# Kernel optimization log

Hardware: AMD Instinct MI355X
Metric: run time of the kernel (lower is better)

Reference implementation:

```python
import jax, jax.numpy as jnp
import numpy as np

NEG_SLOPE = 0.2  # PyG GATConv default negative_slope


def gat_conv(x, src, dst, W, a_src, a_dst, b):
    """PyG GATConv with concat=False (mean over heads). src/dst include self-loops."""
    N = x.shape[0]
    H, C = a_src.shape
    h = (x @ W).reshape(N, H, C)                      # [N,H,C]
    alpha_src = (h * a_src).sum(-1)                   # [N,H]
    alpha_dst = (h * a_dst).sum(-1)                   # [N,H]
    e = jax.nn.leaky_relu(alpha_src[src] + alpha_dst[dst], NEG_SLOPE)  # [E,H]
    # segment softmax over incoming edges of each dst node
    emax = jax.ops.segment_max(e, dst, num_segments=N)                 # [N,H]
    ex = jnp.exp(e - emax[dst])                                        # [E,H]
    denom = jax.ops.segment_sum(ex, dst, num_segments=N)               # [N,H]
    alpha = ex / denom[dst]                                            # [E,H]
    msg = h[src] * alpha[:, :, None]                                   # [E,H,C]
    out = jax.ops.segment_sum(msg, dst, num_segments=N)                # [N,H,C]
    return out.mean(axis=1) + b                                        # concat=False -> mean heads


def setup_inputs() -> dict:
    key = jax.random.key(0)
    ks = jax.random.split(key, 16)
    N, F_IN, H, C, E = 50000, 3, 4, 64, 800000
    inp = {
        "x": jax.random.normal(ks[0], (N, F_IN), dtype=jnp.float32),
        "edge_index": jax.random.randint(ks[1], (2, E), 0, N, dtype=jnp.int32),
        "W1": jax.random.normal(ks[2], (F_IN, H * C), dtype=jnp.float32) * 0.1,
        "a1_src": jax.random.normal(ks[3], (H, C), dtype=jnp.float32) * 0.1,
        "a1_dst": jax.random.normal(ks[4], (H, C), dtype=jnp.float32) * 0.1,
        "b1": jnp.zeros((C,), dtype=jnp.float32),
        "W2": jax.random.normal(ks[5], (C, H * C), dtype=jnp.float32) * 0.1,
        "a2_src": jax.random.normal(ks[6], (H, C), dtype=jnp.float32) * 0.1,
        "a2_dst": jax.random.normal(ks[7], (H, C), dtype=jnp.float32) * 0.1,
        "b2": jnp.zeros((C,), dtype=jnp.float32),
        "W3": jax.random.normal(ks[8], (C, H * C), dtype=jnp.float32) * 0.1,
        "a3_src": jax.random.normal(ks[9], (H, C), dtype=jnp.float32) * 0.1,
        "a3_dst": jax.random.normal(ks[10], (H, C), dtype=jnp.float32) * 0.1,
        "b3": jnp.zeros((C,), dtype=jnp.float32),
        "lin_w": jax.random.normal(ks[11], (C, 1), dtype=jnp.float32) * 0.1,
        "lin_b": jnp.zeros((1,), dtype=jnp.float32),
    }
    return inp


def reference(x, edge_index, W1, a1_src, a1_dst, b1, W2, a2_src, a2_dst, b2,
              W3, a3_src, a3_dst, b3, lin_w, lin_b):
    N = x.shape[0]
    loops = jnp.arange(N, dtype=edge_index.dtype)  # PyG add_self_loops=True default
    src = jnp.concatenate([edge_index[0], loops])
    dst = jnp.concatenate([edge_index[1], loops])

    h1 = jax.nn.elu(gat_conv(x, src, dst, W1, a1_src, a1_dst, b1))
    h2 = jax.nn.elu(gat_conv(h1, src, dst, W2, a2_src, a2_dst, b2)) + h1
    h3 = jax.nn.elu(gat_conv(h2, src, dst, W3, a3_src, a3_dst, b3)) + h2
    return h3 @ lin_w + lin_b
```

## Files before the change

### kernel.cpp

```cpp
#include <hip/hip_runtime.h>
#include <math.h>

#define HEADS 4
#define CH 64
#define HC 256

typedef __attribute__((ext_vector_type(8))) short bf16x8;
typedef __attribute__((ext_vector_type(4))) float f32x4;

__device__ __forceinline__ float lrelu(float v) { return v > 0.f ? v : 0.2f * v; }

__device__ __forceinline__ unsigned int f2bf(float f) {
    unsigned int u = __float_as_uint(f);
    u += 0x7fffu + ((u >> 16) & 1u);
    return u >> 16;
}
__device__ __forceinline__ float bf2f(unsigned short u) {
    return __uint_as_float(((unsigned int)u) << 16);
}

__device__ __forceinline__ float4 wave_sum4(float4 v) {
#pragma unroll
    for (int m = 32; m; m >>= 1) {
        v.x += __shfl_xor(v.x, m);
        v.y += __shfl_xor(v.y, m);
        v.z += __shfl_xor(v.z, m);
        v.w += __shfl_xor(v.w, m);
    }
    return v;
}

__global__ void count_kernel(const int* __restrict__ dst, int E, int vec_ok,
                             float scale8, int* __restrict__ deg) {
    int r = blockIdx.x & 7;
    int i = (blockIdx.x >> 3) * blockDim.x + threadIdx.x;
    int e0 = i * 4;
    if (e0 >= E) return;
    int d[4];
    int cnt;
    if (vec_ok && e0 + 3 < E) {
        int4 v = *(const int4*)(dst + e0);
        d[0] = v.x; d[1] = v.y; d[2] = v.z; d[3] = v.w; cnt = 4;
    } else {
        cnt = min(4, E - e0);
        for (int k = 0; k < cnt; ++k) d[k] = dst[e0 + k];
    }
    for (int k = 0; k < cnt; ++k) {
        int rr = min(7, (int)((float)d[k] * scale8));
        if (rr == r) atomicAdd(&deg[d[k]], 1);
    }
}

__global__ void scan_blocks(const int* __restrict__ deg,
                            int* __restrict__ off,
                            int* __restrict__ bsum,
                            const float* __restrict__ x,
                            float4* __restrict__ xq, int N) {
    __shared__ int sh[256];
    int t = threadIdx.x;
    int g = blockIdx.x * 256 + t;
    int v = (g < N) ? deg[g] + 1 : 0;
    if (g < N) xq[g] = make_float4(x[3 * g], x[3 * g + 1], x[3 * g + 2], 0.f);
    sh[t] = v;
    __syncthreads();
    for (int d = 1; d < 256; d <<= 1) {
        int xv = (t >= d) ? sh[t - d] : 0;
        __syncthreads();
        sh[t] += xv;
        __syncthreads();
    }
    if (g < N) off[g] = sh[t] - v;
    if (t == 255) bsum[blockIdx.x] = sh[255];
}

__global__ void scan_bsums(int* __restrict__ bsum, int G,
                           int* __restrict__ total_out) {
    __shared__ int sh[256];
    int t = threadIdx.x;
    int chunk = (G + 255) / 256;
    int lo = t * chunk, hi = min(lo + chunk, G);
    int s = 0;
    for (int i = lo; i < hi; ++i) s += bsum[i];
    sh[t] = s;
    __syncthreads();
    for (int d = 1; d < 256; d <<= 1) {
        int xv = (t >= d) ? sh[t - d] : 0;
        __syncthreads();
        sh[t] += xv;
        __syncthreads();
    }
    int run = (t > 0) ? sh[t - 1] : 0;
    for (int i = lo; i < hi; ++i) { int v = bsum[i]; bsum[i] = run; run += v; }
    if (t == 255) *total_out = sh[255];
}

__global__ void scan_add(int* __restrict__ off, const int* __restrict__ bsum,
                         const int* __restrict__ deg,
                         int* __restrict__ csr_src, int N) {
    int g = blockIdx.x * 256 + threadIdx.x;
    if (g < N) {
        int o = off[g] + bsum[blockIdx.x];
        off[g] = o;
        csr_src[o + deg[g]] = g;
    }
}

__global__ void scatter_kernel(const int* __restrict__ src,
                               const int* __restrict__ dst, int E, int vec_ok,
                               float scale8,
                               const int* __restrict__ off,
                               int* __restrict__ cursor,
                               int* __restrict__ csr_src) {
    int r = blockIdx.x & 7;
    int i = (blockIdx.x >> 3) * blockDim.x + threadIdx.x;
    int e0 = i * 4;
    if (e0 >= E) return;
    int s[4], d[4];
    int cnt;
    if (vec_ok && e0 + 3 < E) {
        int4 sv = *(const int4*)(src + e0);
        int4 dv = *(const int4*)(dst + e0);
        s[0] = sv.x; s[1] = sv.y; s[2] = sv.z; s[3] = sv.w;
        d[0] = dv.x; d[1] = dv.y; d[2] = dv.z; d[3] = dv.w; cnt = 4;
    } else {
        cnt = min(4, E - e0);
        for (int k = 0; k < cnt; ++k) { s[k] = src[e0 + k]; d[k] = dst[e0 + k]; }
    }
    for (int k = 0; k < cnt; ++k) {
        int rr = min(7, (int)((float)d[k] * scale8));
        if (rr != r) continue;
        int p = atomicAdd(&cursor[d[k]], 1);
        csr_src[off[d[k]] + p] = s[k];
    }
}

__device__ __forceinline__ void prep_blk(int b, int t, const float* W,
                                         const float* a_s, const float* a_d,
                                         unsigned short* Wb, float* ws,
                                         float* wd) {
    if (b < 64) {
        Wb[b * 256 + t] = (unsigned short)f2bf(W[(t >> 2) * HC + (t & 3) * CH + b]);
    } else {
        int idx = (b - 64) * 256 + t;
        int which = idx >= 256;
        int i = which ? idx - 256 : idx;
        int k = i >> 2, h = i & 3;
        const float* av = (which ? a_d : a_s) + h * CH;
        const float* Wr = W + (size_t)k * HC + h * CH;
        float s = 0.f;
        for (int c = 0; c < CH; ++c) s += Wr[c] * av[c];
        (which ? wd : ws)[i] = s;
    }
}

__global__ void prep_all(const float* __restrict__ W1,
                         const float* __restrict__ a1s,
                         const float* __restrict__ a1d,
                         float* __restrict__ ws1, float* __restrict__ wd1,
                         const float* __restrict__ W2,
                         const float* __restrict__ a2s,
                         const float* __restrict__ a2d,
                         unsigned short* __restrict__ Wb2,
                         float* __restrict__ ws2, float* __restrict__ wd2,
                         const float* __restrict__ W3,
                         const float* __restrict__ a3s,
                         const float* __restrict__ a3d,
                         unsigned short* __restrict__ Wb3,
                         float* __restrict__ ws3, float* __restrict__ wd3) {
    int b = blockIdx.x, t = threadIdx.x;
    if (b < 66) {
        prep_blk(b, t, W2, a2s, a2d, Wb2, ws2, wd2);
    } else if (b < 132) {
        prep_blk(b - 66, t, W3, a3s, a3d, Wb3, ws3, wd3);
    } else {
        for (int idx = t; idx < 24; idx += blockDim.x) {
            int which = idx >= 12;
            int i = which ? idx - 12 : idx;
            int k = i >> 2, h = i & 3;
            const float* av = (which ? a1d : a1s) + h * CH;
            const float* Wr = W1 + (size_t)k * HC + h * CH;
            float s = 0.f;
            for (int c = 0; c < CH; ++c) s += Wr[c] * av[c];
            (which ? wd1 : ws1)[i] = s;
        }
    }
}

__global__ void agg_kernel(const int* __restrict__ off,
                           const int* __restrict__ csr_src,
                           const unsigned short* __restrict__ xp,
                           const float4* __restrict__ asrc4,
                           const float4* __restrict__ adst4,
                           uint2* __restrict__ zb2, int N) {
    __shared__ float4 exs[4][64];
    __shared__ unsigned int sss[4][64];
    int node = (blockIdx.x * blockDim.x + threadIdx.x) >> 6;
    int w = (threadIdx.x >> 6) & 3;
    int lane = threadIdx.x & 63;
    if (node >= N) return;
    int o0 = off[node], o1 = off[node + 1];
    int deg = o1 - o0;
    float4 ad = adst4[node];

    float l0 = 0.f, l1 = 0.f, l2 = 0.f, l3 = 0.f;
    float z0 = 0.f, z1 = 0.f, z2 = 0.f, z3 = 0.f;
    const char* xpb = (const char*)xp + lane * 2;

    for (int base = 0; base < deg; base += 64) {
        int i = base + lane;
        int s = 0;
        float4 ev = make_float4(-INFINITY, -INFINITY, -INFINITY, -INFINITY);
        if (i < deg) {
            s = csr_src[o0 + i];
            float4 as = asrc4[s];
            ev.x = lrelu(as.x + ad.x);
            ev.y = lrelu(as.y + ad.y);
            ev.z = lrelu(as.z + ad.z);
            ev.w = lrelu(as.w + ad.w);
        }
        float4 ex;
        ex.x = __expf(ev.x);
        ex.y = __expf(ev.y);
        ex.z = __expf(ev.z);
        ex.w = __expf(ev.w);
        float4 ls = wave_sum4(ex);
        l0 += ls.x; l1 += ls.y; l2 += ls.z; l3 += ls.w;
        exs[w][lane] = ex;
        sss[w][lane] = (unsigned)s * 128u;

        int cnt = min(64, deg - base);
#pragma unroll 4
        for (int e = 0; e < cnt; ++e) {
            unsigned soff = sss[w][e];
            float4 exe = exs[w][e];
            float xk = bf2f(*(const unsigned short*)(xpb + soff));
            z0 += exe.x * xk; z1 += exe.y * xk;
            z2 += exe.z * xk; z3 += exe.w * xk;
        }
    }
    float s0 = 0.25f / l0, s1 = 0.25f / l1, s2 = 0.25f / l2, s3 = 0.25f / l3;
    uint2 zo;
    zo.x = f2bf(z0 * s0) | (f2bf(z1 * s1) << 16);
    zo.y = f2bf(z2 * s2) | (f2bf(z3 * s3) << 16);
    zb2[(size_t)node * CH + lane] = zo;
}

__global__ void gemm_mfma(const unsigned short* __restrict__ zb,
                          const unsigned short* __restrict__ Wb,
                          const float* __restrict__ bias,
                          const float* __restrict__ residual,
                          const float4* __restrict__ wsn4,
                          const float4* __restrict__ wdn4,
                          float4* __restrict__ asrc4,
                          float4* __restrict__ adst4,
                          const float* __restrict__ lin_w,
                          const float* __restrict__ lin_b,
                          float* __restrict__ out_f32,
                          unsigned short* __restrict__ out_pack,
                          float* __restrict__ out_final, int N) {
    int w = threadIdx.x >> 6;
    int lane = threadIdx.x & 63;
    int quad = lane >> 4, col = lane & 15;
    int nbase = blockIdx.x * 64 + w * 16;

    f32x4 zero4 = {0.f, 0.f, 0.f, 0.f};
    f32x4 acc[4];
#pragma unroll
    for (int t = 0; t < 4; ++t) acc[t] = zero4;

    const unsigned short* arow = zb + (size_t)(nbase + col) * HC + quad * 8;
#pragma unroll
    for (int q = 0; q < 8; ++q) {
        bf16x8 af = *(const bf16x8*)(arow + q * 32);
#pragma unroll
        for (int t = 0; t < 4; ++t) {
            const unsigned short* bp = Wb + (size_t)(t * 16 + col) * HC + q * 32 + quad * 8;
            bf16x8 bfrag = *(const bf16x8*)bp;
            acc[t] = __builtin_amdgcn_mfma_f32_16x16x32_bf16(af, bfrag, acc[t], 0, 0, 0);
        }
    }

    if (!out_final) {
        float vv[4][4];
#pragma unroll
        for (int t = 0; t < 4; ++t) {
            int c = t * 16 + col;
            float bc = bias[c];
#pragma unroll
            for (int r = 0; r < 4; ++r) {
                int n = nbase + quad * 4 + r;
                float v = acc[t][r] + bc;
                v = v > 0.f ? v : expm1f(v);
                v += residual[(size_t)n * CH + c];
                vv[t][r] = v;
                if (n < N) {
                    out_f32[(size_t)n * CH + c] = v;
                    out_pack[(size_t)n * CH + c] = (unsigned short)f2bf(v);
                }
            }
        }
        float4 wsv[4], wdv[4];
#pragma unroll
        for (int t = 0; t < 4; ++t) { wsv[t] = wsn4[t * 16 + col]; wdv[t] = wdn4[t * 16 + col]; }
#pragma unroll
        for (int r = 0; r < 4; ++r) {
            int n = nbase + quad * 4 + r;
            float4 sa = make_float4(0.f, 0.f, 0.f, 0.f);
            float4 da = make_float4(0.f, 0.f, 0.f, 0.f);
#pragma unroll
            for (int t = 0; t < 4; ++t) {
                float v = vv[t][r];
                sa.x += v * wsv[t].x; sa.y += v * wsv[t].y;
                sa.z += v * wsv[t].z; sa.w += v * wsv[t].w;
                da.x += v * wdv[t].x; da.y += v * wdv[t].y;
                da.z += v * wdv[t].z; da.w += v * wdv[t].w;
            }
#pragma unroll
            for (int m = 8; m; m >>= 1) {
                sa.x += __shfl_xor(sa.x, m); sa.y += __shfl_xor(sa.y, m);
                sa.z += __shfl_xor(sa.z, m); sa.w += __shfl_xor(sa.w, m);
                da.x += __shfl_xor(da.x, m); da.y += __shfl_xor(da.y, m);
                da.z += __shfl_xor(da.z, m); da.w += __shfl_xor(da.w, m);
            }
            if (col == 0 && n < N) { asrc4[n] = sa; adst4[n] = da; }
        }
    } else {
        float lw[4], bb[4];
#pragma unroll
        for (int t = 0; t < 4; ++t) { lw[t] = lin_w[t * 16 + col]; bb[t] = bias[t * 16 + col]; }
#pragma unroll
        for (int r = 0; r < 4; ++r) {
            int n = nbase + quad * 4 + r;
            float ts = 0.f;
#pragma unroll
            for (int t = 0; t < 4; ++t) {
                float v = acc[t][r] + bb[t];
                v = v > 0.f ? v : expm1f(v);
                v += residual[(size_t)n * CH + (t * 16 + col)];
                ts += v * lw[t];
            }
            ts += __shfl_xor(ts, 1);
            ts += __shfl_xor(ts, 2);
            ts += __shfl_xor(ts, 4);
            ts += __shfl_xor(ts, 8);
            if (col == 0 && n < N) out_final[n] = ts + lin_b[0];
        }
    }
}

__global__ void fused1_kernel(const int* __restrict__ off,
                              const int* __restrict__ csr_src,
                              const float4* __restrict__ xq,
                              const float* __restrict__ ws,
                              const float* __restrict__ wd,
                              float4* __restrict__ zl, int N) {
    int t = blockIdx.x * blockDim.x + threadIdx.x;
    int n = t >> 2, j = t & 3;
    if (n >= N) return;
    float4 xn = xq[n];
    float ad0 = xn.x * wd[0] + xn.y * wd[4] + xn.z * wd[8];
    float ad1 = xn.x * wd[1] + xn.y * wd[5] + xn.z * wd[9];
    float ad2 = xn.x * wd[2] + xn.y * wd[6] + xn.z * wd[10];
    float ad3 = xn.x * wd[3] + xn.y * wd[7] + xn.z * wd[11];

    int o0 = off[n], o1 = off[n + 1];
    float z[12];
#pragma unroll
    for (int q = 0; q < 12; ++q) z[q] = 0.f;
    float l0 = 0.f, l1 = 0.f, l2 = 0.f, l3 = 0.f;

    for (int i = o0 + j; i < o1; i += 4) {
        int s = csr_src[i];
        float4 xv = xq[s];
        float e0 = __expf(lrelu(xv.x * ws[0] + xv.y * ws[4] + xv.z * ws[8]  + ad0));
        float e1 = __expf(lrelu(xv.x * ws[1] + xv.y * ws[5] + xv.z * ws[9]  + ad1));
        float e2 = __expf(lrelu(xv.x * ws[2] + xv.y * ws[6] + xv.z * ws[10] + ad2));
        float e3 = __expf(lrelu(xv.x * ws[3] + xv.y * ws[7] + xv.z * ws[11] + ad3));
        l0 += e0; l1 += e1; l2 += e2; l3 += e3;
        z[0] += e0 * xv.x; z[1]  += e0 * xv.y; z[2]  += e0 * xv.z;
        z[3] += e1 * xv.x; z[4]  += e1 * xv.y; z[5]  += e1 * xv.z;
        z[6] += e2 * xv.x; z[7]  += e2 * xv.y; z[8]  += e2 * xv.z;
        z[9] += e3 * xv.x; z[10] += e3 * xv.y; z[11] += e3 * xv.z;
    }
#pragma unroll
    for (int m = 1; m < 4; m <<= 1) {
#pragma unroll
        for (int q = 0; q < 12; ++q) z[q] += __shfl_xor(z[q], m);
        l0 += __shfl_xor(l0, m);
        l1 += __shfl_xor(l1, m);
        l2 += __shfl_xor(l2, m);
        l3 += __shfl_xor(l3, m);
    }
    if (j == 0) {
        zl[(size_t)n * 4 + 0] = make_float4(z[0], z[1], z[2], z[3]);
        zl[(size_t)n * 4 + 1] = make_float4(z[4], z[5], z[6], z[7]);
        zl[(size_t)n * 4 + 2] = make_float4(z[8], z[9], z[10], z[11]);
        zl[(size_t)n * 4 + 3] = make_float4(l0, l1, l2, l3);
    }
}

__global__ void epi1_kernel(const float4* __restrict__ zl,
                            const float* __restrict__ W1,
                            const float* __restrict__ b1,
                            const float4* __restrict__ ws2_4,
                            const float4* __restrict__ wd2_4,
                            float4* __restrict__ asrc4,
                            float4* __restrict__ adst4,
                            float* __restrict__ out,
                            unsigned short* __restrict__ out_pack, int N) {
    int node = (blockIdx.x * blockDim.x + threadIdx.x) >> 6;
    int c = threadIdx.x & 63;
    if (node >= N) return;
    float4 z0 = zl[(size_t)node * 4 + 0];
    float4 z1 = zl[(size_t)node * 4 + 1];
    float4 z2 = zl[(size_t)node * 4 + 2];
    float4 l4 = zl[(size_t)node * 4 + 3];
    float i0 = 0.25f / l4.x, i1 = 0.25f / l4.y;
    float i2 = 0.25f / l4.z, i3 = 0.25f / l4.w;
    float acc =
        (z0.x * W1[0 * HC +   0 + c] + z0.y * W1[1 * HC +   0 + c] + z0.z * W1[2 * HC +   0 + c]) * i0 +
        (z0.w * W1[0 * HC +  64 + c] + z1.x * W1[1 * HC +  64 + c] + z1.y * W1[2 * HC +  64 + c]) * i1 +
        (z1.z * W1[0 * HC + 128 + c] + z1.w * W1[1 * HC + 128 + c] + z2.x * W1[2 * HC + 128 + c]) * i2 +
        (z2.y * W1[0 * HC + 192 + c] + z2.z * W1[1 * HC + 192 + c] + z2.w * W1[2 * HC + 192 + c]) * i3;
    float v = acc + b1[c];
    v = v > 0.f ? v : expm1f(v);
    out[(size_t)node * CH + c] = v;
    out_pack[(size_t)node * CH + c] = (unsigned short)f2bf(v);
    float4 wsv = ws2_4[c], wdv = wd2_4[c];
    float4 sacc = make_float4(v * wsv.x, v * wsv.y, v * wsv.z, v * wsv.w);
    float4 dacc = make_float4(v * wdv.x, v * wdv.y, v * wdv.z, v * wdv.w);
    sacc = wave_sum4(sacc);
    dacc = wave_sum4(dacc);
    if (c == 0) { asrc4[node] = sacc; adst4[node] = dacc; }
}

extern "C" void kernel_launch(void* const* d_in, const int* in_sizes, int n_in,
                              void* d_out, int out_size, void* d_ws, size_t ws_size,
                              hipStream_t stream) {
    const float* x      = (const float*)d_in[0];
    const int*   ei     = (const int*)  d_in[1];
    const float* W1     = (const float*)d_in[2];
    const float* a1s    = (const float*)d_in[3];
    const float* a1d    = (const float*)d_in[4];
    const float* b1     = (const float*)d_in[5];
    const float* W2     = (const float*)d_in[6];
    const float* a2s    = (const float*)d_in[7];
    const float* a2d    = (const float*)d_in[8];
    const float* b2     = (const float*)d_in[9];
    const float* W3     = (const float*)d_in[10];
    const float* a3s    = (const float*)d_in[11];
    const float* a3d    = (const float*)d_in[12];
    const float* b3     = (const float*)d_in[13];
    const float* lin_w  = (const float*)d_in[14];
    const float* lin_b  = (const float*)d_in[15];

    const int N = in_sizes[0] / 3;
    const int E = in_sizes[1] / 2;
    const int Et = E + N;
    const int* src = ei;
    const int* dst = ei + E;
    const float scale8 = 8.0f / (float)N;
    const int vec_ok = ((((size_t)src | (size_t)dst) & 15) == 0) ? 1 : 0;

    float* xq_f   = (float*)d_ws;
    unsigned short* zb  = (unsigned short*)(xq_f + (size_t)N * 4);
    unsigned short* xpA = zb  + (size_t)N * HC;
    unsigned short* xpB = xpA + (size_t)N * CH;
    unsigned short* Wb2 = xpB + (size_t)N * CH;
    unsigned short* Wb3 = Wb2 + 16384;
    float* bufA   = (float*)(Wb3 + 16384);
    float* bufB   = bufA + (size_t)N * CH;
    float* zl     = bufB + (size_t)N * CH;
    float* asrc   = zl   + (size_t)N * 16;
    float* adst   = asrc + (size_t)N * 4;
    float* ws1    = adst + (size_t)N * 4;
    float* wd1    = ws1 + 16;
    float* ws2    = wd1 + 16;
    float* wd2    = ws2 + 256;
    float* ws3    = wd2 + 256;
    float* wd3    = ws3 + 256;
    int* deg      = (int*)(wd3 + 256);
    int* cursor   = deg + N;
    int* off      = cursor + N;
    int* bsum     = off + N + 4;
    int* csr_src  = bsum + 256;

    const int B = 256;
    const int G = (N + 255) / 256;
    const int EB4 = (E + 3) / 4;
    const int CB = (EB4 + B - 1) / B;

    hipMemsetAsync(deg, 0, (size_t)2 * N * sizeof(int), stream);
    count_kernel<<<CB * 8, B, 0, stream>>>(dst, E, vec_ok, scale8, deg);
    scan_blocks<<<G, B, 0, stream>>>(deg, off, bsum, x, (float4*)xq_f, N);
    scan_bsums<<<1, B, 0, stream>>>(bsum, G, off + N);
    scan_add<<<G, B, 0, stream>>>(off, bsum, deg, csr_src, N);
    scatter_kernel<<<CB * 8, B, 0, stream>>>(src, dst, E, vec_ok, scale8,
                                             off, cursor, csr_src);

    prep_all<<<133, B, 0, stream>>>(W1, a1s, a1d, ws1, wd1,
                                    W2, a2s, a2d, Wb2, ws2, wd2,
                                    W3, a3s, a3d, Wb3, ws3, wd3);

    int nwave_blocks = (N * 64 + B - 1) / B;
    int ngemm_blocks = (N + 63) / 64;

    fused1_kernel<<<(N * 4 + B - 1) / B, B, 0, stream>>>(
        off, csr_src, (const float4*)xq_f, ws1, wd1, (float4*)zl, N);
    epi1_kernel<<<nwave_blocks, B, 0, stream>>>(
        (const float4*)zl, W1, b1, (const float4*)ws2, (const float4*)wd2,
        (float4*)asrc, (float4*)adst, bufA, xpA, N);

    agg_kernel<<<nwave_blocks, B, 0, stream>>>(
        off, csr_src, xpA, (const float4*)asrc, (const float4*)adst,
        (uint2*)zb, N);
    gemm_mfma<<<ngemm_blocks, B, 0, stream>>>(
        zb, Wb2, b2, bufA, (const float4*)ws3, (const float4*)wd3,
        (float4*)asrc, (float4*)adst,
        nullptr, nullptr, bufB, xpB, nullptr, N);

    agg_kernel<<<nwave_blocks, B, 0, stream>>>(
        off, csr_src, xpB, (const float4*)asrc, (const float4*)adst,
        (uint2*)zb, N);
    gemm_mfma<<<ngemm_blocks, B, 0, stream>>>(
        zb, Wb3, b3, bufB, nullptr, nullptr, nullptr, nullptr,
        lin_w, lin_b, nullptr, nullptr, (float*)d_out, N);
}
```

Measured before the change: 344.5 us.

## Reuse count atomics for CSR scatter, fuse layer-1 epilogue, split agg edges across half-waves

The count kernel now stores each edge's atomic slot, so the scatter becomes a plain non-atomic single-pass write instead of an 8-way partitioned atomic pass. The layer-1 aggregation and its epilogue (W1 projection, ELU, attention logits) merge into one kernel, removing the intermediate buffer and a launch. The aggregation kernel processes two edges per step across half-waves with 32-bit two-channel loads, then combines the halves with a shuffle. The cost is an extra E-sized slot array and more registers per lane in aggregation.

```diff
diff --git a/kernel.cpp b/kernel.cpp
--- a/kernel.cpp
+++ b/kernel.cpp
@@ -31,7 +31,8 @@
 }
 
 __global__ void count_kernel(const int* __restrict__ dst, int E, int vec_ok,
-                             float scale8, int* __restrict__ deg) {
+                             float scale8, int* __restrict__ deg,
+                             int* __restrict__ slot) {
     int r = blockIdx.x & 7;
     int i = (blockIdx.x >> 3) * blockDim.x + threadIdx.x;
     int e0 = i * 4;
@@ -47,7 +48,7 @@
     }
     for (int k = 0; k < cnt; ++k) {
         int rr = min(7, (int)((float)d[k] * scale8));
-        if (rr == r) atomicAdd(&deg[d[k]], 1);
+        if (rr == r) slot[e0 + k] = atomicAdd(&deg[d[k]], 1);
     }
 }
 
@@ -105,32 +106,28 @@
     }
 }
 
-__global__ void scatter_kernel(const int* __restrict__ src,
-                               const int* __restrict__ dst, int E, int vec_ok,
-                               float scale8,
-                               const int* __restrict__ off,
-                               int* __restrict__ cursor,
-                               int* __restrict__ csr_src) {
-    int r = blockIdx.x & 7;
-    int i = (blockIdx.x >> 3) * blockDim.x + threadIdx.x;
+__global__ void scatter_plain(const int* __restrict__ src,
+                              const int* __restrict__ dst,
+                              const int* __restrict__ slot, int E, int vec_ok,
+                              const int* __restrict__ off,
+                              int* __restrict__ csr_src) {
+    int i = blockIdx.x * blockDim.x + threadIdx.x;
     int e0 = i * 4;
     if (e0 >= E) return;
-    int s[4], d[4];
-    int cnt;
     if (vec_ok && e0 + 3 < E) {
         int4 sv = *(const int4*)(src + e0);
         int4 dv = *(const int4*)(dst + e0);
-        s[0] = sv.x; s[1] = sv.y; s[2] = sv.z; s[3] = sv.w;
-        d[0] = dv.x; d[1] = dv.y; d[2] = dv.z; d[3] = dv.w; cnt = 4;
+        int4 pv = *(const int4*)(slot + e0);
+        csr_src[off[dv.x] + pv.x] = sv.x;
+        csr_src[off[dv.y] + pv.y] = sv.y;
+        csr_src[off[dv.z] + pv.z] = sv.z;
+        csr_src[off[dv.w] + pv.w] = sv.w;
     } else {
-        cnt = min(4, E - e0);
-        for (int k = 0; k < cnt; ++k) { s[k] = src[e0 + k]; d[k] = dst[e0 + k]; }
-    }
-    for (int k = 0; k < cnt; ++k) {
-        int rr = min(7, (int)((float)d[k] * scale8));
-        if (rr != r) continue;
-        int p = atomicAdd(&cursor[d[k]], 1);
-        csr_src[off[d[k]] + p] = s[k];
+        int cnt = min(4, E - e0);
+        for (int k = 0; k < cnt; ++k) {
+            int e = e0 + k;
+            csr_src[off[dst[e]] + slot[e]] = src[e];
+        }
     }
 }
 
@@ -191,20 +188,24 @@
                            const unsigned short* __restrict__ xp,
                            const float4* __restrict__ asrc4,
                            const float4* __restrict__ adst4,
-                           uint2* __restrict__ zb2, int N) {
+                           unsigned short* __restrict__ zb, int N) {
     __shared__ float4 exs[4][64];
     __shared__ unsigned int sss[4][64];
     int node = (blockIdx.x * blockDim.x + threadIdx.x) >> 6;
     int w = (threadIdx.x >> 6) & 3;
     int lane = threadIdx.x & 63;
     if (node >= N) return;
+    int half = lane >> 5;
+    int lk = lane & 31;
     int o0 = off[node], o1 = off[node + 1];
     int deg = o1 - o0;
     float4 ad = adst4[node];
 
     float l0 = 0.f, l1 = 0.f, l2 = 0.f, l3 = 0.f;
-    float z0 = 0.f, z1 = 0.f, z2 = 0.f, z3 = 0.f;
-    const char* xpb = (const char*)xp + lane * 2;
+    float z[8];
+#pragma unroll
+    for (int q = 0; q < 8; ++q) z[q] = 0.f;
+    const char* xpb2 = (const char*)xp + lk * 4;
 
     for (int base = 0; base < deg; base += 64) {
         int i = base + lane;
@@ -229,20 +230,32 @@
         sss[w][lane] = (unsigned)s * 128u;
 
         int cnt = min(64, deg - base);
-#pragma unroll 4
-        for (int e = 0; e < cnt; ++e) {
+#pragma unroll 2
+        for (int e2 = 0; e2 < cnt; e2 += 2) {
+            int e = e2 + half;
             unsigned soff = sss[w][e];
             float4 exe = exs[w][e];
-            float xk = bf2f(*(const unsigned short*)(xpb + soff));
-            z0 += exe.x * xk; z1 += exe.y * xk;
-            z2 += exe.z * xk; z3 += exe.w * xk;
-        }
-    }
+            unsigned xx = *(const unsigned*)(xpb2 + soff);
+            float xk0 = bf2f((unsigned short)(xx & 0xffffu));
+            float xk1 = bf2f((unsigned short)(xx >> 16));
+            z[0] += exe.x * xk0; z[1] += exe.y * xk0;
+            z[2] += exe.z * xk0; z[3] += exe.w * xk0;
+            z[4] += exe.x * xk1; z[5] += exe.y * xk1;
+            z[6] += exe.z * xk1; z[7] += exe.w * xk1;
+        }
+    }
+#pragma unroll
+    for (int q = 0; q < 8; ++q) z[q] += __shfl_xor(z[q], 32);
+
     float s0 = 0.25f / l0, s1 = 0.25f / l1, s2 = 0.25f / l2, s3 = 0.25f / l3;
-    uint2 zo;
-    zo.x = f2bf(z0 * s0) | (f2bf(z1 * s1) << 16);
-    zo.y = f2bf(z2 * s2) | (f2bf(z3 * s3) << 16);
-    zb2[(size_t)node * CH + lane] = zo;
+    if (half == 0) {
+        uint4 zo;
+        zo.x = f2bf(z[0] * s0) | (f2bf(z[1] * s1) << 16);
+        zo.y = f2bf(z[2] * s2) | (f2bf(z[3] * s3) << 16);
+        zo.z = f2bf(z[4] * s0) | (f2bf(z[5] * s1) << 16);
+        zo.w = f2bf(z[6] * s2) | (f2bf(z[7] * s3) << 16);
+        *(uint4*)((char*)zb + (size_t)node * 512 + lk * 16) = zo;
+    }
 }
 
 __global__ void gemm_mfma(const unsigned short* __restrict__ zb,
@@ -348,12 +361,19 @@
     }
 }
 
-__global__ void fused1_kernel(const int* __restrict__ off,
+__global__ void layer1_kernel(const int* __restrict__ off,
                               const int* __restrict__ csr_src,
                               const float4* __restrict__ xq,
                               const float* __restrict__ ws,
                               const float* __restrict__ wd,
-                              float4* __restrict__ zl, int N) {
+                              const float* __restrict__ W1,
+                              const float* __restrict__ b1,
+                              const float4* __restrict__ ws2_4,
+                              const float4* __restrict__ wd2_4,
+                              float4* __restrict__ asrc4,
+                              float4* __restrict__ adst4,
+                              float* __restrict__ out,
+                              unsigned short* __restrict__ out_pack, int N) {
     int t = blockIdx.x * blockDim.x + threadIdx.x;
     int n = t >> 2, j = t & 3;
     if (n >= N) return;
@@ -391,47 +411,57 @@
         l2 += __shfl_xor(l2, m);
         l3 += __shfl_xor(l3, m);
     }
-    if (j == 0) {
-        zl[(size_t)n * 4 + 0] = make_float4(z[0], z[1], z[2], z[3]);
-        zl[(size_t)n * 4 + 1] = make_float4(z[4], z[5], z[6], z[7]);
-        zl[(size_t)n * 4 + 2] = make_float4(z[8], z[9], z[10], z[11]);
-        zl[(size_t)n * 4 + 3] = make_float4(l0, l1, l2, l3);
-    }
-}
-
-__global__ void epi1_kernel(const float4* __restrict__ zl,
-                            const float* __restrict__ W1,
-                            const float* __restrict__ b1,
-                            const float4* __restrict__ ws2_4,
-                            const float4* __restrict__ wd2_4,
-                            float4* __restrict__ asrc4,
-                            float4* __restrict__ adst4,
-                            float* __restrict__ out,
-                            unsigned short* __restrict__ out_pack, int N) {
-    int node = (blockIdx.x * blockDim.x + threadIdx.x) >> 6;
-    int c = threadIdx.x & 63;
-    if (node >= N) return;
-    float4 z0 = zl[(size_t)node * 4 + 0];
-    float4 z1 = zl[(size_t)node * 4 + 1];
-    float4 z2 = zl[(size_t)node * 4 + 2];
-    float4 l4 = zl[(size_t)node * 4 + 3];
-    float i0 = 0.25f / l4.x, i1 = 0.25f / l4.y;
-    float i2 = 0.25f / l4.z, i3 = 0.25f / l4.w;
-    float acc =
-        (z0.x * W1[0 * HC +   0 + c] + z0.y * W1[1 * HC +   0 + c] + z0.z * W1[2 * HC +   0 + c]) * i0 +
-        (z0.w * W1[0 * HC +  64 + c] + z1.x * W1[1 * HC +  64 + c] + z1.y * W1[2 * HC +  64 + c]) * i1 +
-        (z1.z * W1[0 * HC + 128 + c] + z1.w * W1[1 * HC + 128 + c] + z2.x * W1[2 * HC + 128 + c]) * i2 +
-        (z2.y * W1[0 * HC + 192 + c] + z2.z * W1[1 * HC + 192 + c] + z2.w * W1[2 * HC + 192 + c]) * i3;
-    float v = acc + b1[c];
-    v = v > 0.f ? v : expm1f(v);
-    out[(size_t)node * CH + c] = v;
-    out_pack[(size_t)node * CH + c] = (unsigned short)f2bf(v);
-    float4 wsv = ws2_4[c], wdv = wd2_4[c];
-    float4 sacc = make_float4(v * wsv.x, v * wsv.y, v * wsv.z, v * wsv.w);
-    float4 dacc = make_float4(v * wdv.x, v * wdv.y, v * wdv.z, v * wdv.w);
-    sacc = wave_sum4(sacc);
-    dacc = wave_sum4(dacc);
-    if (c == 0) { asrc4[node] = sacc; adst4[node] = dacc; }
+    float ih[4];
+    ih[0] = 0.25f / l0; ih[1] = 0.25f / l1; ih[2] = 0.25f / l2; ih[3] = 0.25f / l3;
+
+    float4 sacc = make_float4(0.f, 0.f, 0.f, 0.f);
+    float4 dacc = make_float4(0.f, 0.f, 0.f, 0.f);
+    float* orow = out + (size_t)n * CH + j * 16;
+    unsigned short* prow = out_pack + (size_t)n * CH + j * 16;
+#pragma unroll
+    for (int g = 0; g < 4; ++g) {
+        int cbase = j * 16 + g * 4;
+        float4 a = *(const float4*)(b1 + cbase);
+#pragma unroll
+        for (int h = 0; h < 4; ++h) {
+#pragma unroll
+            for (int r = 0; r < 3; ++r) {
+                float4 wv = *(const float4*)(W1 + r * HC + h * 64 + cbase);
+                float zz = z[h * 3 + r] * ih[h];
+                a.x += zz * wv.x; a.y += zz * wv.y;
+                a.z += zz * wv.z; a.w += zz * wv.w;
+            }
+        }
+        float v0 = a.x > 0.f ? a.x : expm1f(a.x);
+        float v1 = a.y > 0.f ? a.y : expm1f(a.y);
+        float v2 = a.z > 0.f ? a.z : expm1f(a.z);
+        float v3 = a.w > 0.f ? a.w : expm1f(a.w);
+        *(float4*)(orow + g * 4) = make_float4(v0, v1, v2, v3);
+        uint2 pk;
+        pk.x = f2bf(v0) | (f2bf(v1) << 16);
+        pk.y = f2bf(v2) | (f2bf(v3) << 16);
+        *(uint2*)(prow + g * 4) = pk;
+        float4 w0 = ws2_4[cbase], w1 = ws2_4[cbase + 1];
+        float4 w2 = ws2_4[cbase + 2], w3 = ws2_4[cbase + 3];
+        sacc.x += v0 * w0.x + v1 * w1.x + v2 * w2.x + v3 * w3.x;
+        sacc.y += v0 * w0.y + v1 * w1.y + v2 * w2.y + v3 * w3.y;
+        sacc.z += v0 * w0.z + v1 * w1.z + v2 * w2.z + v3 * w3.z;
+        sacc.w += v0 * w0.w + v1 * w1.w + v2 * w2.w + v3 * w3.w;
+        float4 d0 = wd2_4[cbase], d1 = wd2_4[cbase + 1];
+        float4 d2 = wd2_4[cbase + 2], d3 = wd2_4[cbase + 3];
+        dacc.x += v0 * d0.x + v1 * d1.x + v2 * d2.x + v3 * d3.x;
+        dacc.y += v0 * d0.y + v1 * d1.y + v2 * d2.y + v3 * d3.y;
+        dacc.z += v0 * d0.z + v1 * d1.z + v2 * d2.z + v3 * d3.z;
+        dacc.w += v0 * d0.w + v1 * d1.w + v2 * d2.w + v3 * d3.w;
+    }
+#pragma unroll
+    for (int m = 1; m < 4; m <<= 1) {
+        sacc.x += __shfl_xor(sacc.x, m); sacc.y += __shfl_xor(sacc.y, m);
+        sacc.z += __shfl_xor(sacc.z, m); sacc.w += __shfl_xor(sacc.w, m);
+        dacc.x += __shfl_xor(dacc.x, m); dacc.y += __shfl_xor(dacc.y, m);
+        dacc.z += __shfl_xor(dacc.z, m); dacc.w += __shfl_xor(dacc.w, m);
+    }
+    if (j == 0) { asrc4[n] = sacc; adst4[n] = dacc; }
 }
 
 extern "C" void kernel_launch(void* const* d_in, const int* in_sizes, int n_in,
@@ -470,8 +500,7 @@
     unsigned short* Wb3 = Wb2 + 16384;
     float* bufA   = (float*)(Wb3 + 16384);
     float* bufB   = bufA + (size_t)N * CH;
-    float* zl     = bufB + (size_t)N * CH;
-    float* asrc   = zl   + (size_t)N * 16;
+    float* asrc   = bufB + (size_t)N * CH;
     float* adst   = asrc + (size_t)N * 4;
     float* ws1    = adst + (size_t)N * 4;
     float* wd1    = ws1 + 16;
@@ -480,23 +509,22 @@
     float* ws3    = wd2 + 256;
     float* wd3    = ws3 + 256;
     int* deg      = (int*)(wd3 + 256);
-    int* cursor   = deg + N;
-    int* off      = cursor + N;
+    int* off      = deg + N;
     int* bsum     = off + N + 4;
-    int* csr_src  = bsum + 256;
+    int* slot     = bsum + 256;
+    int* csr_src  = slot + E;
 
     const int B = 256;
     const int G = (N + 255) / 256;
     const int EB4 = (E + 3) / 4;
     const int CB = (EB4 + B - 1) / B;
 
-    hipMemsetAsync(deg, 0, (size_t)2 * N * sizeof(int), stream);
-    count_kernel<<<CB * 8, B, 0, stream>>>(dst, E, vec_ok, scale8, deg);
+    hipMemsetAsync(deg, 0, (size_t)N * sizeof(int), stream);
+    count_kernel<<<CB * 8, B, 0, stream>>>(dst, E, vec_ok, scale8, deg, slot);
     scan_blocks<<<G, B, 0, stream>>>(deg, off, bsum, x, (float4*)xq_f, N);
     scan_bsums<<<1, B, 0, stream>>>(bsum, G, off + N);
     scan_add<<<G, B, 0, stream>>>(off, bsum, deg, csr_src, N);
-    scatter_kernel<<<CB * 8, B, 0, stream>>>(src, dst, E, vec_ok, scale8,
-                                             off, cursor, csr_src);
+    scatter_plain<<<CB, B, 0, stream>>>(src, dst, slot, E, vec_ok, off, csr_src);
 
     prep_all<<<133, B, 0, stream>>>(W1, a1s, a1d, ws1, wd1,
                                     W2, a2s, a2d, Wb2, ws2, wd2,
@@ -505,15 +533,14 @@
     int nwave_blocks = (N * 64 + B - 1) / B;
     int ngemm_blocks = (N + 63) / 64;
 
-    fused1_kernel<<<(N * 4 + B - 1) / B, B, 0, stream>>>(
-        off, csr_src, (const float4*)xq_f, ws1, wd1, (float4*)zl, N);
-    epi1_kernel<<<nwave_blocks, B, 0, stream>>>(
-        (const float4*)zl, W1, b1, (const float4*)ws2, (const float4*)wd2,
+    layer1_kernel<<<(N * 4 + B - 1) / B, B, 0, stream>>>(
+        off, csr_src, (const float4*)xq_f, ws1, wd1, W1, b1,
+        (const float4*)ws2, (const float4*)wd2,
         (float4*)asrc, (float4*)adst, bufA, xpA, N);
 
     agg_kernel<<<nwave_blocks, B, 0, stream>>>(
         off, csr_src, xpA, (const float4*)asrc, (const float4*)adst,
-        (uint2*)zb, N);
+        zb, N);
     gemm_mfma<<<ngemm_blocks, B, 0, stream>>>(
         zb, Wb2, b2, bufA, (const float4*)ws3, (const float4*)wd3,
         (float4*)asrc, (float4*)adst,
@@ -521,7 +548,7 @@
 
     agg_kernel<<<nwave_blocks, B, 0, stream>>>(
         off, csr_src, xpB, (const float4*)asrc, (const float4*)adst,
-        (uint2*)zb, N);
+        zb, N);
     gemm_mfma<<<ngemm_blocks, B, 0, stream>>>(
         zb, Wb3, b3, bufB, nullptr, nullptr, nullptr, nullptr,
         lin_w, lin_b, nullptr, nullptr, (float*)d_out, N);
```

Result: faster. 335.1 us (-2.7%).
